# Performance work log

Hardware: AMD Instinct MI355X
Metric: run time of the kernel (lower is better)

The kernel has to match this reference:

```python
import jax, jax.numpy as jnp
import numpy as np

N = 100000
IN_DIM = 128
HID = 128
HEADS = 2
OUT_DIM = 2
E = 800000
NEG_SLOPE = 0.2


def setup_inputs() -> dict:
    key = jax.random.key(0)
    ks = jax.random.split(key, 12)
    x = jax.random.normal(ks[0], (N, IN_DIM), dtype=jnp.float32)
    edge_index = jax.random.randint(ks[1], (2, E), 0, N, dtype=jnp.int64)
    s = 0.05
    # GATConv layer 1: in=128 -> heads=2, out=128
    W1 = jax.random.normal(ks[2], (IN_DIM, HEADS * HID), dtype=jnp.float32) * s
    a_src1 = jax.random.normal(ks[3], (HEADS, HID), dtype=jnp.float32) * s
    a_dst1 = jax.random.normal(ks[4], (HEADS, HID), dtype=jnp.float32) * s
    b1 = jnp.zeros((HEADS * HID,), dtype=jnp.float32)
    # GATConv layer 2: in=256 -> heads=2, out=128
    W2 = jax.random.normal(ks[5], (HEADS * HID, HEADS * HID), dtype=jnp.float32) * s
    a_src2 = jax.random.normal(ks[6], (HEADS, HID), dtype=jnp.float32) * s
    a_dst2 = jax.random.normal(ks[7], (HEADS, HID), dtype=jnp.float32) * s
    b2 = jnp.zeros((HEADS * HID,), dtype=jnp.float32)
    # post_mp: Linear(256,128) -> Dropout(eval, no-op) -> Linear(128,2)
    Wp1 = jax.random.normal(ks[8], (HEADS * HID, HID), dtype=jnp.float32) * s
    bp1 = jnp.zeros((HID,), dtype=jnp.float32)
    Wp2 = jax.random.normal(ks[9], (HID, OUT_DIM), dtype=jnp.float32) * s
    bp2 = jnp.zeros((OUT_DIM,), dtype=jnp.float32)
    return {"x": x, "edge_index": edge_index,
            "W1": W1, "a_src1": a_src1, "a_dst1": a_dst1, "b1": b1,
            "W2": W2, "a_src2": a_src2, "a_dst2": a_dst2, "b2": b2,
            "Wp1": Wp1, "bp1": bp1, "Wp2": Wp2, "bp2": bp2}


def gat_conv(x, src, dst, W, a_src, a_dst, b):
    # linear transform, split heads: [N, H, C]
    h = (x @ W).reshape(-1, HEADS, HID)
    # per-node attention logits: [N, H]
    alpha_src = jnp.sum(h * a_src, axis=-1)
    alpha_dst = jnp.sum(h * a_dst, axis=-1)
    # per-edge logits, edge e = (src -> dst): [E, H]
    e = jax.nn.leaky_relu(alpha_src[src] + alpha_dst[dst], NEG_SLOPE)
    # segment softmax over incoming edges of each destination node
    m = jax.ops.segment_max(e, dst, num_segments=N)
    e = jnp.exp(e - m[dst])
    denom = jax.ops.segment_sum(e, dst, num_segments=N)
    alpha = e / (denom[dst] + 1e-16)
    # gather source features, weight, scatter-add to destinations
    msg = h[src] * alpha[:, :, None]            # [E, H, C]
    out = jax.ops.segment_sum(msg, dst, num_segments=N)  # [N, H, C]
    return out.reshape(-1, HEADS * HID) + b


def reference(x, edge_index, W1, a_src1, a_dst1, b1, W2, a_src2, a_dst2, b2,
              Wp1, bp1, Wp2, bp2):
    # add self-loops (PyG GATConv default)
    loops = jnp.arange(N, dtype=edge_index.dtype)
    src = jnp.concatenate([edge_index[0], loops])
    dst = jnp.concatenate([edge_index[1], loops])
    h = jax.nn.relu(gat_conv(x, src, dst, W1, a_src1, a_dst1, b1))
    h = jax.nn.relu(gat_conv(h, src, dst, W2, a_src2, a_dst2, b2))
    h = h @ Wp1 + bp1          # post_mp Linear 1 (dropout is eval no-op)
    h = h @ Wp2 + bp2          # post_mp Linear 2
    return jax.nn.sigmoid(h)
```

## Files before the change

kernel.cpp:

```cpp
#include <hip/hip_runtime.h>
#include <hip/hip_bf16.h>
#include <math.h>

#define NNODES 100000
#define NPAD   100032
#define IN_DIM 128
#define HID 128
#define HEADS 2
#define F2 256
#define NEDGES 800000
#define ETOT 900000
#define NEG_SLOPE 0.2f

typedef unsigned int uint;
typedef unsigned short ushort;
typedef __attribute__((ext_vector_type(8))) short short8;
typedef __attribute__((ext_vector_type(4))) float floatx4;

__device__ __forceinline__ ushort f2bf(float f) {
    uint u = __builtin_bit_cast(uint, f);
    u += 0x7fffu + ((u >> 16) & 1u);
    return (ushort)(u >> 16);
}
__device__ __forceinline__ float bf2f(uint u16) {
    return __builtin_bit_cast(float, u16 << 16);
}
__device__ __forceinline__ float wred_sum(float v) {
    for (int o = 32; o; o >>= 1) v += __shfl_xor(v, o);
    return v;
}

__global__ __launch_bounds__(256) void hist_kernel(const int* __restrict__ ei,
                                                   int* __restrict__ deg) {
    int i = blockIdx.x * 256 + threadIdx.x;
    if (i >= ETOT) return;
    int dst = (i < NEDGES) ? ei[NEDGES + i] : (i - NEDGES);
    atomicAdd(&deg[dst], 1);
}

__global__ __launch_bounds__(256) void scan1_kernel(const int* __restrict__ deg,
                                                    int* __restrict__ row_start,
                                                    int* __restrict__ bsum) {
    __shared__ int s[256];
    int t = threadIdx.x;
    int i = blockIdx.x * 256 + t;
    int v = (i < NNODES) ? deg[i] : 0;
    s[t] = v;
    __syncthreads();
    for (int off = 1; off < 256; off <<= 1) {
        int x = (t >= off) ? s[t - off] : 0;
        __syncthreads();
        s[t] += x;
        __syncthreads();
    }
    if (i < NNODES) row_start[i] = s[t] - v;
    if (t == 255) bsum[blockIdx.x] = s[255];
}

__global__ __launch_bounds__(512) void scan2_kernel(const int* __restrict__ bsum,
                                                    int* __restrict__ bsum2,
                                                    int cnt) {
    __shared__ int s[512];
    int t = threadIdx.x;
    int v = (t < cnt) ? bsum[t] : 0;
    s[t] = v;
    __syncthreads();
    for (int off = 1; off < 512; off <<= 1) {
        int x = (t >= off) ? s[t - off] : 0;
        __syncthreads();
        s[t] += x;
        __syncthreads();
    }
    bsum2[t] = s[t] - v;
}

__global__ __launch_bounds__(256) void scan3_kernel(int* __restrict__ row_start,
                                                    const int* __restrict__ bsum2,
                                                    int* __restrict__ cursor) {
    int i = blockIdx.x * 256 + threadIdx.x;
    if (i == 0) row_start[NNODES] = ETOT;
    if (i >= NNODES) return;
    int r = row_start[i] + bsum2[i >> 8];
    row_start[i] = r;
    cursor[i] = r;
}

__global__ __launch_bounds__(256) void scatter_kernel(const int* __restrict__ ei,
                                                      int* __restrict__ cursor,
                                                      int* __restrict__ csr_src) {
    int i = blockIdx.x * 256 + threadIdx.x;
    if (i >= ETOT) return;
    int src, dst;
    if (i < NEDGES) { src = ei[i]; dst = ei[NEDGES + i]; }
    else            { src = i - NEDGES; dst = src; }
    int pos = atomicAdd(&cursor[dst], 1);
    csr_src[pos] = src;
}

__global__ __launch_bounds__(256) void transpose_bf_kernel(const float* __restrict__ W,
                                                           ushort* __restrict__ Wt,
                                                           int K, int N) {
    int i = blockIdx.x * 256 + threadIdx.x;
    if (i >= K * N) return;
    int n = i / K, k = i - n * K;
    Wt[(size_t)n * K + k] = f2bf(W[(size_t)k * N + n]);
}

__global__ __launch_bounds__(256) void fw_kernel(const float* __restrict__ Wp1,
                                                 const float* __restrict__ bp1,
                                                 const float* __restrict__ Wp2,
                                                 const float* __restrict__ bp2,
                                                 float2* __restrict__ Wf,
                                                 float* __restrict__ bfv) {
    int k = threadIdx.x;
    float s0 = 0.f, s1 = 0.f;
    for (int m = 0; m < 128; m++) {
        float w = Wp1[(size_t)k * 128 + m];
        s0 += w * Wp2[2 * m];
        s1 += w * Wp2[2 * m + 1];
    }
    Wf[k] = make_float2(s0, s1);
    if (k < 2) {
        float b = bp2[k];
        for (int m = 0; m < 128; m++) b += bp1[m] * Wp2[2 * m + k];
        bfv[k] = b;
    }
}

__global__ __launch_bounds__(256) void mfma_gemm_f32A(const float* __restrict__ A,
                                                      const ushort* __restrict__ Bt,
                                                      ushort* __restrict__ C,
                                                      float* __restrict__ as_f,
                                                      float* __restrict__ ad_f,
                                                      const float* __restrict__ aS,
                                                      const float* __restrict__ aD,
                                                      int N, int K) {
    __shared__ ushort As[64][40];
    __shared__ ushort Bs[64][40];
    int t = threadIdx.x;
    int wave = t >> 6, lane = t & 63;
    int quad = lane >> 4, l16 = lane & 15;
    size_t rowBase = (size_t)blockIdx.x * 64;
    int colBase = blockIdx.y * 64;

    floatx4 acc[4];
#pragma unroll
    for (int i = 0; i < 4; i++) acc[i] = (floatx4){0.f, 0.f, 0.f, 0.f};

    int ar = t >> 2, ac = (t & 3) * 8;
    int agr = (int)rowBase + ar;
    const float*  Ap = A + (size_t)agr * K + ac;
    const ushort* Bp = Bt + (size_t)(colBase + ar) * K + ac;
    bool aok = agr < NNODES;

    for (int k0 = 0; k0 < K; k0 += 32) {
        float4 f0 = make_float4(0.f, 0.f, 0.f, 0.f), f1 = f0;
        if (aok) {
            f0 = *reinterpret_cast<const float4*>(Ap + k0);
            f1 = *reinterpret_cast<const float4*>(Ap + k0 + 4);
        }
        uint4 bv = *reinterpret_cast<const uint4*>(Bp + k0);
        uint u0 = (uint)f2bf(f0.x) | ((uint)f2bf(f0.y) << 16);
        uint u1 = (uint)f2bf(f0.z) | ((uint)f2bf(f0.w) << 16);
        uint u2 = (uint)f2bf(f1.x) | ((uint)f2bf(f1.y) << 16);
        uint u3 = (uint)f2bf(f1.z) | ((uint)f2bf(f1.w) << 16);
        *reinterpret_cast<uint2*>(&As[ar][ac])     = make_uint2(u0, u1);
        *reinterpret_cast<uint2*>(&As[ar][ac + 4]) = make_uint2(u2, u3);
        *reinterpret_cast<uint2*>(&Bs[ar][ac])     = make_uint2(bv.x, bv.y);
        *reinterpret_cast<uint2*>(&Bs[ar][ac + 4]) = make_uint2(bv.z, bv.w);
        __syncthreads();

        union { uint2 u[2]; short8 s; } afr, bfr;
        afr.u[0] = *reinterpret_cast<const uint2*>(&As[wave * 16 + l16][quad * 8]);
        afr.u[1] = *reinterpret_cast<const uint2*>(&As[wave * 16 + l16][quad * 8 + 4]);
#pragma unroll
        for (int nt = 0; nt < 4; nt++) {
            bfr.u[0] = *reinterpret_cast<const uint2*>(&Bs[nt * 16 + l16][quad * 8]);
            bfr.u[1] = *reinterpret_cast<const uint2*>(&Bs[nt * 16 + l16][quad * 8 + 4]);
            acc[nt] = __builtin_amdgcn_mfma_f32_16x16x32_bf16(afr.s, bfr.s, acc[nt], 0, 0, 0);
        }
        __syncthreads();
    }

#pragma unroll
    for (int nt = 0; nt < 4; nt++) {
        int col = colBase + nt * 16 + l16;
#pragma unroll
        for (int r = 0; r < 4; r++) {
            size_t row = rowBase + wave * 16 + quad * 4 + r;
            C[row * N + col] = f2bf(acc[nt][r]);
        }
    }
    int head = colBase >> 7;
#pragma unroll
    for (int r = 0; r < 4; r++) {
        float ps = 0.f, pd = 0.f;
#pragma unroll
        for (int nt = 0; nt < 4; nt++) {
            int c = colBase + nt * 16 + l16;
            ps += acc[nt][r] * aS[c];
            pd += acc[nt][r] * aD[c];
        }
#pragma unroll
        for (int o = 1; o < 16; o <<= 1) {
            ps += __shfl_xor(ps, o);
            pd += __shfl_xor(pd, o);
        }
        if (l16 == 0) {
            size_t row = rowBase + wave * 16 + quad * 4 + r;
            atomicAdd(&as_f[2 * row + head], ps);
            atomicAdd(&ad_f[2 * row + head], pd);
        }
    }
}

__global__ __launch_bounds__(256) void mfma_gemm_bf16A(const ushort* __restrict__ A,
                                                       const ushort* __restrict__ Bt,
                                                       ushort* __restrict__ C,
                                                       float* __restrict__ as_f,
                                                       float* __restrict__ ad_f,
                                                       const float* __restrict__ aS,
                                                       const float* __restrict__ aD,
                                                       int N, int K) {
    __shared__ ushort As[64][40];
    __shared__ ushort Bs[64][40];
    int t = threadIdx.x;
    int wave = t >> 6, lane = t & 63;
    int quad = lane >> 4, l16 = lane & 15;
    size_t rowBase = (size_t)blockIdx.x * 64;
    int colBase = blockIdx.y * 64;

    floatx4 acc[4];
#pragma unroll
    for (int i = 0; i < 4; i++) acc[i] = (floatx4){0.f, 0.f, 0.f, 0.f};

    int ar = t >> 2, ac = (t & 3) * 8;
    const ushort* Ap = A + ((size_t)blockIdx.x * 64 + ar) * K + ac;
    const ushort* Bp = Bt + (size_t)(colBase + ar) * K + ac;

    for (int k0 = 0; k0 < K; k0 += 32) {
        uint4 av = *reinterpret_cast<const uint4*>(Ap + k0);
        uint4 bv = *reinterpret_cast<const uint4*>(Bp + k0);
        *reinterpret_cast<uint2*>(&As[ar][ac])     = make_uint2(av.x, av.y);
        *reinterpret_cast<uint2*>(&As[ar][ac + 4]) = make_uint2(av.z, av.w);
        *reinterpret_cast<uint2*>(&Bs[ar][ac])     = make_uint2(bv.x, bv.y);
        *reinterpret_cast<uint2*>(&Bs[ar][ac + 4]) = make_uint2(bv.z, bv.w);
        __syncthreads();

        union { uint2 u[2]; short8 s; } afr, bfr;
        afr.u[0] = *reinterpret_cast<const uint2*>(&As[wave * 16 + l16][quad * 8]);
        afr.u[1] = *reinterpret_cast<const uint2*>(&As[wave * 16 + l16][quad * 8 + 4]);
#pragma unroll
        for (int nt = 0; nt < 4; nt++) {
            bfr.u[0] = *reinterpret_cast<const uint2*>(&Bs[nt * 16 + l16][quad * 8]);
            bfr.u[1] = *reinterpret_cast<const uint2*>(&Bs[nt * 16 + l16][quad * 8 + 4]);
            acc[nt] = __builtin_amdgcn_mfma_f32_16x16x32_bf16(afr.s, bfr.s, acc[nt], 0, 0, 0);
        }
        __syncthreads();
    }

#pragma unroll
    for (int nt = 0; nt < 4; nt++) {
        int col = colBase + nt * 16 + l16;
#pragma unroll
        for (int r = 0; r < 4; r++) {
            size_t row = rowBase + wave * 16 + quad * 4 + r;
            C[row * N + col] = f2bf(acc[nt][r]);
        }
    }
    int head = colBase >> 7;
#pragma unroll
    for (int r = 0; r < 4; r++) {
        float ps = 0.f, pd = 0.f;
#pragma unroll
        for (int nt = 0; nt < 4; nt++) {
            int c = colBase + nt * 16 + l16;
            ps += acc[nt][r] * aS[c];
            pd += acc[nt][r] * aD[c];
        }
#pragma unroll
        for (int o = 1; o < 16; o <<= 1) {
            ps += __shfl_xor(ps, o);
            pd += __shfl_xor(pd, o);
        }
        if (l16 == 0) {
            size_t row = rowBase + wave * 16 + quad * 4 + r;
            atomicAdd(&as_f[2 * row + head], ps);
            atomicAdd(&ad_f[2 * row + head], pd);
        }
    }
}

__device__ __forceinline__ float edge_w(float2 q, float2 ad, int hsel) {
    float l = hsel ? (q.y + ad.y) : (q.x + ad.x);
    l = l > 0.f ? l : NEG_SLOPE * l;
    return __expf(l);
}

__global__ __launch_bounds__(256) void gather_kernel(const uint2* __restrict__ hb2,
                                                     const int* __restrict__ row_start,
                                                     const int* __restrict__ csr_src,
                                                     const float2* __restrict__ as_,
                                                     const float2* __restrict__ ad_,
                                                     const float4* __restrict__ bias4,
                                                     uint2* __restrict__ outb2) {
    int wave = threadIdx.x >> 6, lane = threadIdx.x & 63;
    int n = blockIdx.x * 4 + wave;
    if (n >= NNODES) return;
    int beg = row_start[n], end = row_start[n + 1];
    float2 ad = ad_[n];
    int hsel = lane >> 5;
    float a0 = 0.f, a1 = 0.f, a2 = 0.f, a3 = 0.f, den = 0.f;

    int j = beg;
    for (; j + 3 < end; j += 4) {
        int s0 = csr_src[j],     s1 = csr_src[j + 1];
        int s2 = csr_src[j + 2], s3 = csr_src[j + 3];
        float2 q0 = as_[s0], q1 = as_[s1], q2 = as_[s2], q3 = as_[s3];
        uint2 h0 = hb2[(size_t)s0 * 64 + lane];
        uint2 h1 = hb2[(size_t)s1 * 64 + lane];
        uint2 h2 = hb2[(size_t)s2 * 64 + lane];
        uint2 h3 = hb2[(size_t)s3 * 64 + lane];
        float w0 = edge_w(q0, ad, hsel), w1 = edge_w(q1, ad, hsel);
        float w2 = edge_w(q2, ad, hsel), w3 = edge_w(q3, ad, hsel);
        den += (w0 + w1) + (w2 + w3);
        a0 += w0 * bf2f(h0.x & 0xffffu) + w1 * bf2f(h1.x & 0xffffu)
            + w2 * bf2f(h2.x & 0xffffu) + w3 * bf2f(h3.x & 0xffffu);
        a1 += w0 * bf2f(h0.x >> 16) + w1 * bf2f(h1.x >> 16)
            + w2 * bf2f(h2.x >> 16) + w3 * bf2f(h3.x >> 16);
        a2 += w0 * bf2f(h0.y & 0xffffu) + w1 * bf2f(h1.y & 0xffffu)
            + w2 * bf2f(h2.y & 0xffffu) + w3 * bf2f(h3.y & 0xffffu);
        a3 += w0 * bf2f(h0.y >> 16) + w1 * bf2f(h1.y >> 16)
            + w2 * bf2f(h2.y >> 16) + w3 * bf2f(h3.y >> 16);
    }
    for (; j < end; j++) {
        int s = csr_src[j];
        float2 q = as_[s];
        uint2 hv = hb2[(size_t)s * 64 + lane];
        float w = edge_w(q, ad, hsel);
        den += w;
        a0 += w * bf2f(hv.x & 0xffffu);
        a1 += w * bf2f(hv.x >> 16);
        a2 += w * bf2f(hv.y & 0xffffu);
        a3 += w * bf2f(hv.y >> 16);
    }
    float inv = 1.f / (den + 1e-16f);
    float4 b = bias4[lane];
    float o0 = fmaxf(a0 * inv + b.x, 0.f);
    float o1 = fmaxf(a1 * inv + b.y, 0.f);
    float o2 = fmaxf(a2 * inv + b.z, 0.f);
    float o3 = fmaxf(a3 * inv + b.w, 0.f);
    uint2 pk;
    pk.x = (uint)f2bf(o0) | ((uint)f2bf(o1) << 16);
    pk.y = (uint)f2bf(o2) | ((uint)f2bf(o3) << 16);
    outb2[(size_t)n * 64 + lane] = pk;
}

__global__ __launch_bounds__(256) void gemv_kernel(const uint* __restrict__ hb2,
                                                   const float2* __restrict__ Wf,
                                                   const float* __restrict__ bfv,
                                                   float* __restrict__ out) {
    int wave = threadIdx.x >> 6, lane = threadIdx.x & 63;
    int n = blockIdx.x * 4 + wave;
    if (n >= NNODES) return;
    uint2 p = reinterpret_cast<const uint2*>(hb2 + (size_t)n * 128)[lane];
    float f0 = bf2f(p.x & 0xffffu), f1 = bf2f(p.x >> 16);
    float f2 = bf2f(p.y & 0xffffu), f3 = bf2f(p.y >> 16);
    float4 wa = reinterpret_cast<const float4*>(Wf)[2 * lane];
    float4 wb = reinterpret_cast<const float4*>(Wf)[2 * lane + 1];
    float p0 = wred_sum(f0 * wa.x + f1 * wa.z + f2 * wb.x + f3 * wb.z);
    float p1 = wred_sum(f0 * wa.y + f1 * wa.w + f2 * wb.y + f3 * wb.w);
    if (lane == 0) {
        out[2 * n]     = 1.f / (1.f + __expf(-(p0 + bfv[0])));
        out[2 * n + 1] = 1.f / (1.f + __expf(-(p1 + bfv[1])));
    }
}

extern "C" void kernel_launch(void* const* d_in, const int* in_sizes, int n_in,
                              void* d_out, int out_size, void* d_ws, size_t ws_size,
                              hipStream_t stream) {
    const float* x      = (const float*)d_in[0];
    const int*   ei     = (const int*)d_in[1];
    const float* W1     = (const float*)d_in[2];
    const float* a_src1 = (const float*)d_in[3];
    const float* a_dst1 = (const float*)d_in[4];
    const float* b1     = (const float*)d_in[5];
    const float* W2     = (const float*)d_in[6];
    const float* a_src2 = (const float*)d_in[7];
    const float* a_dst2 = (const float*)d_in[8];
    const float* b2     = (const float*)d_in[9];
    const float* Wp1    = (const float*)d_in[10];
    const float* bp1    = (const float*)d_in[11];
    const float* Wp2    = (const float*)d_in[12];
    const float* bp2    = (const float*)d_in[13];
    float* outp = (float*)d_out;

    char* w = (char*)d_ws;
    ushort* hbf  = (ushort*)w; w += (size_t)NPAD * 256 * sizeof(ushort);
    ushort* obf  = (ushort*)w; w += (size_t)NPAD * 256 * sizeof(ushort);
    ushort* W1t  = (ushort*)w; w += (size_t)256 * 128 * sizeof(ushort);
    ushort* W2t  = (ushort*)w; w += (size_t)256 * 256 * sizeof(ushort);
    float2* Wf   = (float2*)w; w += 256 * sizeof(float2);
    float*  bfv  = (float*)w;  w += 4 * sizeof(float);
    float2* as_  = (float2*)w; w += (size_t)NPAD * sizeof(float2);
    float2* ad_  = (float2*)w; w += (size_t)NPAD * sizeof(float2);
    int* deg       = (int*)w; w += (size_t)NNODES * sizeof(int);
    int* row_start = (int*)w; w += (size_t)(NNODES + 16) * sizeof(int);
    int* cursor    = (int*)w; w += (size_t)NNODES * sizeof(int);
    int* csr_src   = (int*)w; w += (size_t)ETOT * sizeof(int);
    int* bsum      = (int*)w; w += 512 * sizeof(int);
    int* bsum2     = (int*)w; w += 512 * sizeof(int);

    const int SCAN_BLOCKS = (NNODES + 255) / 256;
    const int NODE_WAVES  = (NNODES + 3) / 4;
    const int MB = NPAD / 64;
    const size_t ALPHA_BYTES = 2 * (size_t)NPAD * sizeof(float2);

    hipMemsetAsync(deg, 0, (size_t)NNODES * sizeof(int), stream);
    hist_kernel<<<(ETOT + 255) / 256, 256, 0, stream>>>(ei, deg);
    scan1_kernel<<<SCAN_BLOCKS, 256, 0, stream>>>(deg, row_start, bsum);
    scan2_kernel<<<1, 512, 0, stream>>>(bsum, bsum2, SCAN_BLOCKS);
    scan3_kernel<<<SCAN_BLOCKS, 256, 0, stream>>>(row_start, bsum2, cursor);
    scatter_kernel<<<(ETOT + 255) / 256, 256, 0, stream>>>(ei, cursor, csr_src);

    transpose_bf_kernel<<<(128 * 256 + 255) / 256, 256, 0, stream>>>(W1, W1t, 128, 256);
    transpose_bf_kernel<<<(256 * 256 + 255) / 256, 256, 0, stream>>>(W2, W2t, 256, 256);
    fw_kernel<<<1, 256, 0, stream>>>(Wp1, bp1, Wp2, bp2, Wf, bfv);

    hipMemsetAsync(as_, 0, ALPHA_BYTES, stream);
    mfma_gemm_f32A<<<dim3(MB, 4), 256, 0, stream>>>(x, W1t, hbf, (float*)as_, (float*)ad_,
                                                    a_src1, a_dst1, 256, 128);
    gather_kernel<<<NODE_WAVES, 256, 0, stream>>>((const uint2*)hbf, row_start, csr_src,
                                                  as_, ad_, (const float4*)b1, (uint2*)obf);

    hipMemsetAsync(as_, 0, ALPHA_BYTES, stream);
    mfma_gemm_bf16A<<<dim3(MB, 4), 256, 0, stream>>>(obf, W2t, hbf, (float*)as_, (float*)ad_,
                                                     a_src2, a_dst2, 256, 256);
    gather_kernel<<<NODE_WAVES, 256, 0, stream>>>((const uint2*)hbf, row_start, csr_src,
                                                  as_, ad_, (const float4*)b2, (uint2*)obf);

    gemv_kernel<<<NODE_WAVES, 256, 0, stream>>>((const uint*)obf, Wf, bfv, outp);
}
```

Before: 485.3 us.

## Widen GEMM tiles to one head, drop atomics, batch edge weights, fuse final GEMV

The GEMM kernels now compute a full 128-column head per block, so the attention-logit dot products are complete in-block and written with plain stores. This removes the atomics and the two memsets that zeroed their targets. The gather kernel computes edge weights for 64 edges in parallel, one per lane, and broadcasts them with readlane instead of recomputing them per edge. The final post-MLP GEMV and sigmoid are fused into the second gather, which removes a kernel launch and one write and read of the hidden features. The wider tiles use more registers and LDS per block and launch half as many blocks.

```diff
diff --git a/kernel.cpp b/kernel.cpp
--- a/kernel.cpp
+++ b/kernel.cpp
@@ -134,23 +134,25 @@
                                                       float* __restrict__ ad_f,
                                                       const float* __restrict__ aS,
                                                       const float* __restrict__ aD,
-                                                      int N, int K) {
+                                                      int K) {
     __shared__ ushort As[64][40];
-    __shared__ ushort Bs[64][40];
+    __shared__ ushort Bs[128][40];
     int t = threadIdx.x;
     int wave = t >> 6, lane = t & 63;
     int quad = lane >> 4, l16 = lane & 15;
     size_t rowBase = (size_t)blockIdx.x * 64;
-    int colBase = blockIdx.y * 64;
-
-    floatx4 acc[4];
-#pragma unroll
-    for (int i = 0; i < 4; i++) acc[i] = (floatx4){0.f, 0.f, 0.f, 0.f};
+    int colBase = blockIdx.y * 128;
+    int head = blockIdx.y;
+
+    floatx4 acc[8];
+#pragma unroll
+    for (int i = 0; i < 8; i++) acc[i] = (floatx4){0.f, 0.f, 0.f, 0.f};
 
     int ar = t >> 2, ac = (t & 3) * 8;
     int agr = (int)rowBase + ar;
-    const float*  Ap = A + (size_t)agr * K + ac;
-    const ushort* Bp = Bt + (size_t)(colBase + ar) * K + ac;
+    const float*  Ap  = A + (size_t)agr * K + ac;
+    const ushort* Bp0 = Bt + (size_t)(colBase + ar) * K + ac;
+    const ushort* Bp1 = Bp0 + (size_t)64 * K;
     bool aok = agr < NNODES;
 
     for (int k0 = 0; k0 < K; k0 += 32) {
@@ -159,47 +161,51 @@
             f0 = *reinterpret_cast<const float4*>(Ap + k0);
             f1 = *reinterpret_cast<const float4*>(Ap + k0 + 4);
         }
-        uint4 bv = *reinterpret_cast<const uint4*>(Bp + k0);
-        uint u0 = (uint)f2bf(f0.x) | ((uint)f2bf(f0.y) << 16);
-        uint u1 = (uint)f2bf(f0.z) | ((uint)f2bf(f0.w) << 16);
-        uint u2 = (uint)f2bf(f1.x) | ((uint)f2bf(f1.y) << 16);
-        uint u3 = (uint)f2bf(f1.z) | ((uint)f2bf(f1.w) << 16);
-        *reinterpret_cast<uint2*>(&As[ar][ac])     = make_uint2(u0, u1);
-        *reinterpret_cast<uint2*>(&As[ar][ac + 4]) = make_uint2(u2, u3);
-        *reinterpret_cast<uint2*>(&Bs[ar][ac])     = make_uint2(bv.x, bv.y);
-        *reinterpret_cast<uint2*>(&Bs[ar][ac + 4]) = make_uint2(bv.z, bv.w);
-        __syncthreads();
-
-        union { uint2 u[2]; short8 s; } afr, bfr;
-        afr.u[0] = *reinterpret_cast<const uint2*>(&As[wave * 16 + l16][quad * 8]);
-        afr.u[1] = *reinterpret_cast<const uint2*>(&As[wave * 16 + l16][quad * 8 + 4]);
-#pragma unroll
-        for (int nt = 0; nt < 4; nt++) {
-            bfr.u[0] = *reinterpret_cast<const uint2*>(&Bs[nt * 16 + l16][quad * 8]);
-            bfr.u[1] = *reinterpret_cast<const uint2*>(&Bs[nt * 16 + l16][quad * 8 + 4]);
+        uint4 b0 = *reinterpret_cast<const uint4*>(Bp0 + k0);
+        uint4 b1 = *reinterpret_cast<const uint4*>(Bp1 + k0);
+        uint4 av;
+        av.x = (uint)f2bf(f0.x) | ((uint)f2bf(f0.y) << 16);
+        av.y = (uint)f2bf(f0.z) | ((uint)f2bf(f0.w) << 16);
+        av.z = (uint)f2bf(f1.x) | ((uint)f2bf(f1.y) << 16);
+        av.w = (uint)f2bf(f1.z) | ((uint)f2bf(f1.w) << 16);
+        *reinterpret_cast<uint4*>(&As[ar][ac])      = av;
+        *reinterpret_cast<uint4*>(&Bs[ar][ac])      = b0;
+        *reinterpret_cast<uint4*>(&Bs[64 + ar][ac]) = b1;
+        __syncthreads();
+
+        union { uint4 u; short8 s; } afr, bfr;
+        afr.u = *reinterpret_cast<const uint4*>(&As[wave * 16 + l16][quad * 8]);
+#pragma unroll
+        for (int nt = 0; nt < 8; nt++) {
+            bfr.u = *reinterpret_cast<const uint4*>(&Bs[nt * 16 + l16][quad * 8]);
             acc[nt] = __builtin_amdgcn_mfma_f32_16x16x32_bf16(afr.s, bfr.s, acc[nt], 0, 0, 0);
         }
         __syncthreads();
     }
 
 #pragma unroll
-    for (int nt = 0; nt < 4; nt++) {
+    for (int nt = 0; nt < 8; nt++) {
         int col = colBase + nt * 16 + l16;
 #pragma unroll
         for (int r = 0; r < 4; r++) {
             size_t row = rowBase + wave * 16 + quad * 4 + r;
-            C[row * N + col] = f2bf(acc[nt][r]);
-        }
-    }
-    int head = colBase >> 7;
+            C[row * F2 + col] = f2bf(acc[nt][r]);
+        }
+    }
+    float aSv[8], aDv[8];
+#pragma unroll
+    for (int nt = 0; nt < 8; nt++) {
+        int c = colBase + nt * 16 + l16;
+        aSv[nt] = aS[c];
+        aDv[nt] = aD[c];
+    }
 #pragma unroll
     for (int r = 0; r < 4; r++) {
         float ps = 0.f, pd = 0.f;
 #pragma unroll
-        for (int nt = 0; nt < 4; nt++) {
-            int c = colBase + nt * 16 + l16;
-            ps += acc[nt][r] * aS[c];
-            pd += acc[nt][r] * aD[c];
+        for (int nt = 0; nt < 8; nt++) {
+            ps += acc[nt][r] * aSv[nt];
+            pd += acc[nt][r] * aDv[nt];
         }
 #pragma unroll
         for (int o = 1; o < 16; o <<= 1) {
@@ -208,8 +214,8 @@
         }
         if (l16 == 0) {
             size_t row = rowBase + wave * 16 + quad * 4 + r;
-            atomicAdd(&as_f[2 * row + head], ps);
-            atomicAdd(&ad_f[2 * row + head], pd);
+            as_f[2 * row + head] = ps;
+            ad_f[2 * row + head] = pd;
         }
     }
 }
@@ -221,62 +227,67 @@
                                                        float* __restrict__ ad_f,
                                                        const float* __restrict__ aS,
                                                        const float* __restrict__ aD,
-                                                       int N, int K) {
+                                                       int K) {
     __shared__ ushort As[64][40];
-    __shared__ ushort Bs[64][40];
+    __shared__ ushort Bs[128][40];
     int t = threadIdx.x;
     int wave = t >> 6, lane = t & 63;
     int quad = lane >> 4, l16 = lane & 15;
     size_t rowBase = (size_t)blockIdx.x * 64;
-    int colBase = blockIdx.y * 64;
-
-    floatx4 acc[4];
-#pragma unroll
-    for (int i = 0; i < 4; i++) acc[i] = (floatx4){0.f, 0.f, 0.f, 0.f};
+    int colBase = blockIdx.y * 128;
+    int head = blockIdx.y;
+
+    floatx4 acc[8];
+#pragma unroll
+    for (int i = 0; i < 8; i++) acc[i] = (floatx4){0.f, 0.f, 0.f, 0.f};
 
     int ar = t >> 2, ac = (t & 3) * 8;
-    const ushort* Ap = A + ((size_t)blockIdx.x * 64 + ar) * K + ac;
-    const ushort* Bp = Bt + (size_t)(colBase + ar) * K + ac;
+    const ushort* Ap  = A + (rowBase + ar) * K + ac;
+    const ushort* Bp0 = Bt + (size_t)(colBase + ar) * K + ac;
+    const ushort* Bp1 = Bp0 + (size_t)64 * K;
 
     for (int k0 = 0; k0 < K; k0 += 32) {
         uint4 av = *reinterpret_cast<const uint4*>(Ap + k0);
-        uint4 bv = *reinterpret_cast<const uint4*>(Bp + k0);
-        *reinterpret_cast<uint2*>(&As[ar][ac])     = make_uint2(av.x, av.y);
-        *reinterpret_cast<uint2*>(&As[ar][ac + 4]) = make_uint2(av.z, av.w);
-        *reinterpret_cast<uint2*>(&Bs[ar][ac])     = make_uint2(bv.x, bv.y);
-        *reinterpret_cast<uint2*>(&Bs[ar][ac + 4]) = make_uint2(bv.z, bv.w);
-        __syncthreads();
-
-        union { uint2 u[2]; short8 s; } afr, bfr;
-        afr.u[0] = *reinterpret_cast<const uint2*>(&As[wave * 16 + l16][quad * 8]);
-        afr.u[1] = *reinterpret_cast<const uint2*>(&As[wave * 16 + l16][quad * 8 + 4]);
-#pragma unroll
-        for (int nt = 0; nt < 4; nt++) {
-            bfr.u[0] = *reinterpret_cast<const uint2*>(&Bs[nt * 16 + l16][quad * 8]);
-            bfr.u[1] = *reinterpret_cast<const uint2*>(&Bs[nt * 16 + l16][quad * 8 + 4]);
+        uint4 b0 = *reinterpret_cast<const uint4*>(Bp0 + k0);
+        uint4 b1 = *reinterpret_cast<const uint4*>(Bp1 + k0);
+        *reinterpret_cast<uint4*>(&As[ar][ac])      = av;
+        *reinterpret_cast<uint4*>(&Bs[ar][ac])      = b0;
+        *reinterpret_cast<uint4*>(&Bs[64 + ar][ac]) = b1;
+        __syncthreads();
+
+        union { uint4 u; short8 s; } afr, bfr;
+        afr.u = *reinterpret_cast<const uint4*>(&As[wave * 16 + l16][quad * 8]);
+#pragma unroll
+        for (int nt = 0; nt < 8; nt++) {
+            bfr.u = *reinterpret_cast<const uint4*>(&Bs[nt * 16 + l16][quad * 8]);
             acc[nt] = __builtin_amdgcn_mfma_f32_16x16x32_bf16(afr.s, bfr.s, acc[nt], 0, 0, 0);
         }
         __syncthreads();
     }
 
 #pragma unroll
-    for (int nt = 0; nt < 4; nt++) {
+    for (int nt = 0; nt < 8; nt++) {
         int col = colBase + nt * 16 + l16;
 #pragma unroll
         for (int r = 0; r < 4; r++) {
             size_t row = rowBase + wave * 16 + quad * 4 + r;
-            C[row * N + col] = f2bf(acc[nt][r]);
-        }
-    }
-    int head = colBase >> 7;
+            C[row * F2 + col] = f2bf(acc[nt][r]);
+        }
+    }
+    float aSv[8], aDv[8];
+#pragma unroll
+    for (int nt = 0; nt < 8; nt++) {
+        int c = colBase + nt * 16 + l16;
+        aSv[nt] = aS[c];
+        aDv[nt] = aD[c];
+    }
 #pragma unroll
     for (int r = 0; r < 4; r++) {
         float ps = 0.f, pd = 0.f;
 #pragma unroll
-        for (int nt = 0; nt < 4; nt++) {
-            int c = colBase + nt * 16 + l16;
-            ps += acc[nt][r] * aS[c];
-            pd += acc[nt][r] * aD[c];
+        for (int nt = 0; nt < 8; nt++) {
+            ps += acc[nt][r] * aSv[nt];
+            pd += acc[nt][r] * aDv[nt];
         }
 #pragma unroll
         for (int o = 1; o < 16; o <<= 1) {
@@ -285,16 +296,10 @@
         }
         if (l16 == 0) {
             size_t row = rowBase + wave * 16 + quad * 4 + r;
-            atomicAdd(&as_f[2 * row + head], ps);
-            atomicAdd(&ad_f[2 * row + head], pd);
-        }
-    }
-}
-
-__device__ __forceinline__ float edge_w(float2 q, float2 ad, int hsel) {
-    float l = hsel ? (q.y + ad.y) : (q.x + ad.x);
-    l = l > 0.f ? l : NEG_SLOPE * l;
-    return __expf(l);
+            as_f[2 * row + head] = ps;
+            ad_f[2 * row + head] = pd;
+        }
+    }
 }
 
 __global__ __launch_bounds__(256) void gather_kernel(const uint2* __restrict__ hb2,
@@ -303,76 +308,72 @@
                                                      const float2* __restrict__ as_,
                                                      const float2* __restrict__ ad_,
                                                      const float4* __restrict__ bias4,
-                                                     uint2* __restrict__ outb2) {
+                                                     uint2* __restrict__ outb2,
+                                                     const float4* __restrict__ WfA,
+                                                     const float* __restrict__ bfv,
+                                                     float2* __restrict__ outp,
+                                                     int final_mode) {
     int wave = threadIdx.x >> 6, lane = threadIdx.x & 63;
     int n = blockIdx.x * 4 + wave;
     if (n >= NNODES) return;
     int beg = row_start[n], end = row_start[n + 1];
     float2 ad = ad_[n];
-    int hsel = lane >> 5;
-    float a0 = 0.f, a1 = 0.f, a2 = 0.f, a3 = 0.f, den = 0.f;
-
-    int j = beg;
-    for (; j + 3 < end; j += 4) {
-        int s0 = csr_src[j],     s1 = csr_src[j + 1];
-        int s2 = csr_src[j + 2], s3 = csr_src[j + 3];
-        float2 q0 = as_[s0], q1 = as_[s1], q2 = as_[s2], q3 = as_[s3];
-        uint2 h0 = hb2[(size_t)s0 * 64 + lane];
-        uint2 h1 = hb2[(size_t)s1 * 64 + lane];
-        uint2 h2 = hb2[(size_t)s2 * 64 + lane];
-        uint2 h3 = hb2[(size_t)s3 * 64 + lane];
-        float w0 = edge_w(q0, ad, hsel), w1 = edge_w(q1, ad, hsel);
-        float w2 = edge_w(q2, ad, hsel), w3 = edge_w(q3, ad, hsel);
-        den += (w0 + w1) + (w2 + w3);
-        a0 += w0 * bf2f(h0.x & 0xffffu) + w1 * bf2f(h1.x & 0xffffu)
-            + w2 * bf2f(h2.x & 0xffffu) + w3 * bf2f(h3.x & 0xffffu);
-        a1 += w0 * bf2f(h0.x >> 16) + w1 * bf2f(h1.x >> 16)
-            + w2 * bf2f(h2.x >> 16) + w3 * bf2f(h3.x >> 16);
-        a2 += w0 * bf2f(h0.y & 0xffffu) + w1 * bf2f(h1.y & 0xffffu)
-            + w2 * bf2f(h2.y & 0xffffu) + w3 * bf2f(h3.y & 0xffffu);
-        a3 += w0 * bf2f(h0.y >> 16) + w1 * bf2f(h1.y >> 16)
-            + w2 * bf2f(h2.y >> 16) + w3 * bf2f(h3.y >> 16);
-    }
-    for (; j < end; j++) {
-        int s = csr_src[j];
-        float2 q = as_[s];
-        uint2 hv = hb2[(size_t)s * 64 + lane];
-        float w = edge_w(q, ad, hsel);
-        den += w;
-        a0 += w * bf2f(hv.x & 0xffffu);
-        a1 += w * bf2f(hv.x >> 16);
-        a2 += w * bf2f(hv.y & 0xffffu);
-        a3 += w * bf2f(hv.y >> 16);
-    }
-    float inv = 1.f / (den + 1e-16f);
+    bool head1 = lane >= 32;
+
+    float a0 = 0.f, a1 = 0.f, a2 = 0.f, a3 = 0.f;
+    float aden = 0.f;
+
+    for (int chunk = beg; chunk < end; chunk += 64) {
+        int cnt = end - chunk;
+        if (cnt > 64) cnt = 64;
+        int e = chunk + lane;
+        int sv = csr_src[(e < end) ? e : (end - 1)];
+        float2 q = as_[sv];
+        float l0 = q.x + ad.x; l0 = l0 > 0.f ? l0 : NEG_SLOPE * l0;
+        float l1 = q.y + ad.y; l1 = l1 > 0.f ? l1 : NEG_SLOPE * l1;
+        float w0 = __expf(l0);
+        float w1 = __expf(l1);
+
+#pragma unroll 4
+        for (int j = 0; j < cnt; j++) {
+            int   sj  = __builtin_amdgcn_readlane(sv, j);
+            float wj0 = __builtin_bit_cast(float,
+                          __builtin_amdgcn_readlane(__builtin_bit_cast(int, w0), j));
+            float wj1 = __builtin_bit_cast(float,
+                          __builtin_amdgcn_readlane(__builtin_bit_cast(int, w1), j));
+            float wj = head1 ? wj1 : wj0;
+            uint2 hv = hb2[(size_t)sj * 64 + lane];
+            aden += wj;
+            a0 += wj * bf2f(hv.x & 0xffffu);
+            a1 += wj * bf2f(hv.x >> 16);
+            a2 += wj * bf2f(hv.y & 0xffffu);
+            a3 += wj * bf2f(hv.y >> 16);
+        }
+    }
+    float inv = 1.f / (aden + 1e-16f);
     float4 b = bias4[lane];
     float o0 = fmaxf(a0 * inv + b.x, 0.f);
     float o1 = fmaxf(a1 * inv + b.y, 0.f);
     float o2 = fmaxf(a2 * inv + b.z, 0.f);
     float o3 = fmaxf(a3 * inv + b.w, 0.f);
-    uint2 pk;
-    pk.x = (uint)f2bf(o0) | ((uint)f2bf(o1) << 16);
-    pk.y = (uint)f2bf(o2) | ((uint)f2bf(o3) << 16);
-    outb2[(size_t)n * 64 + lane] = pk;
-}
-
-__global__ __launch_bounds__(256) void gemv_kernel(const uint* __restrict__ hb2,
-                                                   const float2* __restrict__ Wf,
-                                                   const float* __restrict__ bfv,
-                                                   float* __restrict__ out) {
-    int wave = threadIdx.x >> 6, lane = threadIdx.x & 63;
-    int n = blockIdx.x * 4 + wave;
-    if (n >= NNODES) return;
-    uint2 p = reinterpret_cast<const uint2*>(hb2 + (size_t)n * 128)[lane];
-    float f0 = bf2f(p.x & 0xffffu), f1 = bf2f(p.x >> 16);
-    float f2 = bf2f(p.y & 0xffffu), f3 = bf2f(p.y >> 16);
-    float4 wa = reinterpret_cast<const float4*>(Wf)[2 * lane];
-    float4 wb = reinterpret_cast<const float4*>(Wf)[2 * lane + 1];
-    float p0 = wred_sum(f0 * wa.x + f1 * wa.z + f2 * wb.x + f3 * wb.z);
-    float p1 = wred_sum(f0 * wa.y + f1 * wa.w + f2 * wb.y + f3 * wb.w);
-    if (lane == 0) {
-        out[2 * n]     = 1.f / (1.f + __expf(-(p0 + bfv[0])));
-        out[2 * n + 1] = 1.f / (1.f + __expf(-(p1 + bfv[1])));
+    if (!final_mode) {
+        uint2 pk;
+        pk.x = (uint)f2bf(o0) | ((uint)f2bf(o1) << 16);
+        pk.y = (uint)f2bf(o2) | ((uint)f2bf(o3) << 16);
+        outb2[(size_t)n * 64 + lane] = pk;
+    } else {
+        float4 wa = WfA[2 * lane];
+        float4 wb = WfA[2 * lane + 1];
+        float p0 = o0 * wa.x + o1 * wa.z + o2 * wb.x + o3 * wb.z;
+        float p1 = o0 * wa.y + o1 * wa.w + o2 * wb.y + o3 * wb.w;
+        p0 = wred_sum(p0);
+        p1 = wred_sum(p1);
+        if (lane == 0) {
+            float2 r;
+            r.x = 1.f / (1.f + __expf(-(p0 + bfv[0])));
+            r.y = 1.f / (1.f + __expf(-(p1 + bfv[1])));
+            outp[n] = r;
+        }
     }
 }
 
@@ -414,7 +415,6 @@
     const int SCAN_BLOCKS = (NNODES + 255) / 256;
     const int NODE_WAVES  = (NNODES + 3) / 4;
     const int MB = NPAD / 64;
-    const size_t ALPHA_BYTES = 2 * (size_t)NPAD * sizeof(float2);
 
     hipMemsetAsync(deg, 0, (size_t)NNODES * sizeof(int), stream);
     hist_kernel<<<(ETOT + 255) / 256, 256, 0, stream>>>(ei, deg);
@@ -427,17 +427,15 @@
     transpose_bf_kernel<<<(256 * 256 + 255) / 256, 256, 0, stream>>>(W2, W2t, 256, 256);
     fw_kernel<<<1, 256, 0, stream>>>(Wp1, bp1, Wp2, bp2, Wf, bfv);
 
-    hipMemsetAsync(as_, 0, ALPHA_BYTES, stream);
-    mfma_gemm_f32A<<<dim3(MB, 4), 256, 0, stream>>>(x, W1t, hbf, (float*)as_, (float*)ad_,
-                                                    a_src1, a_dst1, 256, 128);
+    mfma_gemm_f32A<<<dim3(MB, 2), 256, 0, stream>>>(x, W1t, hbf, (float*)as_, (float*)ad_,
+                                                    a_src1, a_dst1, 128);
     gather_kernel<<<NODE_WAVES, 256, 0, stream>>>((const uint2*)hbf, row_start, csr_src,
-                                                  as_, ad_, (const float4*)b1, (uint2*)obf);
-
-    hipMemsetAsync(as_, 0, ALPHA_BYTES, stream);
-    mfma_gemm_bf16A<<<dim3(MB, 4), 256, 0, stream>>>(obf, W2t, hbf, (float*)as_, (float*)ad_,
-                                                     a_src2, a_dst2, 256, 256);
+                                                  as_, ad_, (const float4*)b1, (uint2*)obf,
+                                                  (const float4*)Wf, bfv, (float2*)outp, 0);
+
+    mfma_gemm_bf16A<<<dim3(MB, 2), 256, 0, stream>>>(obf, W2t, hbf, (float*)as_, (float*)ad_,
+                                                     a_src2, a_dst2, 256);
     gather_kernel<<<NODE_WAVES, 256, 0, stream>>>((const uint2*)hbf, row_start, csr_src,
-                                                  as_, ad_, (const float4*)b2, (uint2*)obf);
-
-    gemv_kernel<<<NODE_WAVES, 256, 0, stream>>>((const uint*)obf, Wf, bfv, outp);
-}
+                                                  as_, ad_, (const float4*)b2, (uint2*)obf,
+                                                  (const float4*)Wf, bfv, (float2*)outp, 1);
+}
```

Result: faster. 448.7 us (-7.6%).
